# Optimization experiments

Measured on AMD Instinct MI355X. Metric: run time of the kernel, lower is better.

Reference implementation:

```python
import jax, jax.numpy as jnp
import numpy as np

N, H, W, M = 1, 128, 128, 16
HID, STY, CIN, NC, COL = 256, 256, 128, 7, 64


def _lrelu(v):
    return jnp.where(v > 0, v, 0.2 * v)


def _conv(x, w, b=None):
    y = jax.lax.conv_general_dilated(x, w, (1, 1), 'SAME',
                                     dimension_numbers=('NCHW', 'OIHW', 'NCHW'))
    return y if b is None else y + b[None, :, None, None]


def _modlin(f, z, Wt, Wa, ba, Wb, bb):
    # ModLinear, bias=False, mod_bias=True, output_mode=True:
    # y = (f * alpha) @ W^T + beta
    alpha = z @ Wa.T + ba          # [N, in]
    beta = z @ Wb.T + bb           # [N, out]
    return jnp.einsum('nsi,oi->nso', f * alpha[:, None, :], Wt) + beta[:, None, :]


def setup_inputs() -> dict:
    key = jax.random.key(0)
    k = jax.random.split(key, 24)
    s = lambda f: np.float32(1.0 / np.sqrt(f))
    inp = {}
    inp['x'] = jax.random.normal(k[0], (N, H, W, M, CIN), jnp.float32)
    inp['m'] = jax.random.uniform(k[1], (N, H, W, M, NC), jnp.float32)
    inp['z'] = jax.random.normal(k[2], (N, STY), jnp.float32)
    inp['dists'] = jax.random.uniform(k[3], (N, H, W, M), jnp.float32) * 0.05
    # RenderMLP params
    inp['w1'] = jax.random.normal(k[4], (HID, CIN)) * s(CIN)
    inp['b1'] = jnp.zeros((HID,), jnp.float32)
    inp['wma'] = jax.random.normal(k[5], (HID, NC)) * s(NC)
    # 5 stacked ModLinears (fc_2, fc_3, fc_4, fc_5, fc_6)
    inp['ml_w'] = jax.random.normal(k[6], (5, HID, HID)) * s(HID)
    inp['ml_wa'] = jax.random.normal(k[7], (5, HID, STY)) * s(STY)
    inp['ml_ba'] = jnp.ones((5, HID), jnp.float32)
    inp['ml_wb'] = jax.random.normal(k[8], (5, HID, STY)) * s(STY)
    inp['ml_bb'] = jnp.zeros((5, HID), jnp.float32)
    inp['wsig'] = jax.random.normal(k[9], (1, HID)) * s(HID)
    inp['bsig'] = jnp.zeros((1,), jnp.float32)
    inp['wc'] = jax.random.normal(k[10], (COL, HID)) * s(HID)
    inp['bc'] = jnp.zeros((COL,), jnp.float32)
    # RenderCNN params
    inp['wz'] = jax.random.normal(k[11], (4 * HID, STY)) * s(STY)
    inp['bz'] = jnp.zeros((4 * HID,), jnp.float32)
    inp['c1_w'] = jax.random.normal(k[12], (HID, COL, 1, 1)) * s(COL)
    inp['c1_b'] = jnp.zeros((HID,), jnp.float32)
    inp['c2a_w'] = jax.random.normal(k[13], (HID, HID, 3, 3)) * s(HID * 9)
    inp['c2a_b'] = jnp.zeros((HID,), jnp.float32)
    inp['c2b_w'] = jax.random.normal(k[14], (HID, HID, 3, 3)) * s(HID * 9)
    inp['c3a_w'] = jax.random.normal(k[15], (HID, HID, 3, 3)) * s(HID * 9)
    inp['c3a_b'] = jnp.zeros((HID,), jnp.float32)
    inp['c3b_w'] = jax.random.normal(k[16], (HID, HID, 3, 3)) * s(HID * 9)
    inp['c4a_w'] = jax.random.normal(k[17], (HID, HID, 1, 1)) * s(HID)
    inp['c4a_b'] = jnp.zeros((HID,), jnp.float32)
    inp['c4b_w'] = jax.random.normal(k[18], (HID, HID, 1, 1)) * s(HID)
    inp['c4b_b'] = jnp.zeros((HID,), jnp.float32)
    inp['c4_w'] = jax.random.normal(k[19], (3, HID, 1, 1)) * s(HID)
    inp['c4_b'] = jnp.zeros((3,), jnp.float32)
    return inp


def reference(x, m, z, dists, w1, b1, wma, ml_w, ml_wa, ml_ba, ml_wb, ml_bb,
              wsig, bsig, wc, bc, wz, bz, c1_w, c1_b, c2a_w, c2a_b, c2b_w,
              c3a_w, c3a_b, c3b_w, c4a_w, c4a_b, c4b_w, c4b_b, c4_w, c4_b):
    n, h, w_, mm, cin = x.shape
    xf = x.reshape(n, -1, cin)              # [N, S, 128], S = H*W*M
    mf = m.reshape(n, -1, m.shape[-1])      # [N, S, 7]
    # RenderMLP
    f = jnp.einsum('nsi,oi->nso', xf, w1) + b1 + jnp.einsum('nsi,oi->nso', mf, wma)
    f = _lrelu(f)
    for i in range(3):  # fc_2, fc_3, fc_4
        f = _lrelu(_modlin(f, z, ml_w[i], ml_wa[i], ml_ba[i], ml_wb[i], ml_bb[i]))
    sigma = jnp.einsum('nsi,oi->nso', f, wsig) + bsig   # [N, S, 1]
    for i in (3, 4):    # fc_5, fc_6
        f = _lrelu(_modlin(f, z, ml_w[i], ml_wa[i], ml_ba[i], ml_wb[i], ml_bb[i]))
    c = jnp.einsum('nsi,oi->nso', f, wc) + bc           # [N, S, 64]
    # Volumetric alpha compositing along the M ray samples
    sigma = sigma.reshape(n, h, w_, mm)
    c = c.reshape(n, h, w_, mm, -1)
    alpha = 1.0 - jnp.exp(-jax.nn.relu(sigma) * dists)  # [N,H,W,M]
    t = jnp.cumprod(1.0 - alpha + 1e-10, axis=-1)
    t_excl = jnp.concatenate([jnp.ones_like(t[..., :1]), t[..., :-1]], axis=-1)
    wgt = alpha * t_excl
    feat = jnp.einsum('nhwm,nhwmc->nchw', wgt, c)       # [N, 64, H, W]
    # RenderCNN with style modulation
    zc = z @ wz.T + bz
    a0, a1, a2, a3 = jnp.split(zc, 4, axis=-1)
    mod = lambda y, wm, bm: y * (wm[:, :, None, None] + 1.0) + bm[:, :, None, None]
    y = _lrelu(_conv(feat, c1_w, c1_b))
    y = y + _conv(_lrelu(_conv(y, c2a_w, c2a_b)), c2b_w)
    y = _lrelu(mod(y, a0, a1))
    y = y + _conv(_lrelu(_conv(y, c3a_w, c3a_b)), c3b_w)
    y = _lrelu(mod(y, a2, a3))
    y = y + _conv(_lrelu(_conv(y, c4a_w, c4a_b)), c4b_w, c4b_b)
    y = _lrelu(y)
    return _conv(y, c4_w, c4_b)  # [N, 3, H, W]
```

## Files before the change

### kernel.cpp

```cpp
#include <hip/hip_runtime.h>
#include <hip/hip_bf16.h>

#define NPIX 16384
#define S_TOT 262144

typedef __attribute__((ext_vector_type(8))) short bf16x8;
typedef __attribute__((ext_vector_type(4))) float f32x4;

__device__ __forceinline__ float lrelu(float v) { return v > 0.f ? v : 0.2f * v; }
__device__ __forceinline__ unsigned short f2b(float f) {
  unsigned u = __float_as_uint(f);
  return (unsigned short)((u + 0x7FFFu + ((u >> 16) & 1u)) >> 16);
}
__device__ __forceinline__ unsigned pk2(float a, float b) {
  return (unsigned)f2b(a) | ((unsigned)f2b(b) << 16);
}
__device__ __forceinline__ float b2f(short s) {
  return __uint_as_float(((unsigned)(unsigned short)s) << 16);
}
__device__ __forceinline__ float f_lo(int u) { return __uint_as_float((unsigned)u << 16); }
__device__ __forceinline__ float f_hi(int u) { return __uint_as_float((unsigned)u & 0xffff0000u); }

__device__ float g_alpha[5 * 256];
__device__ float g_beta[5 * 256];
__device__ float g_amod[1024];
__device__ float g_sigma[S_TOT];
__device__ float g_c[S_TOT * 64];
__device__ short g_featb[NPIX * 64];
__device__ short g_y1[NPIX * 256];
__device__ short g_y2[NPIX * 256];
__device__ short g_y3[NPIX * 256];
__device__ short g_t [NPIX * 256];
__device__ short g_wpack[385024];
#define O_C1  0
#define O_C2A 16384
#define O_C2B (16384 + 589824)
#define O_C3A (16384 + 2 * 589824)
#define O_C3B (16384 + 3 * 589824)
#define O_C4A (16384 + 4 * 589824)
#define O_C4B (16384 + 4 * 589824 + 65536)
__device__ short g_wpack2[2506752];

__global__ __launch_bounds__(256) void kparams(const float* __restrict__ z,
    const float* __restrict__ wa, const float* __restrict__ ba,
    const float* __restrict__ wb, const float* __restrict__ bb,
    const float* __restrict__ wz, const float* __restrict__ bz) {
  __shared__ float zs[256];
  const int t = threadIdx.x;
  zs[t] = z[t];
  __syncthreads();
  for (int l = 0; l < 5; ++l) {
    float accA = ba[l * 256 + t];
    float accB = bb[l * 256 + t];
    const float* rowA = wa + (l * 256 + t) * 256;
    const float* rowB = wb + (l * 256 + t) * 256;
    for (int k = 0; k < 256; k += 4) {
      float4 va = *(const float4*)(rowA + k);
      float4 vb = *(const float4*)(rowB + k);
      accA += va.x * zs[k] + va.y * zs[k + 1] + va.z * zs[k + 2] + va.w * zs[k + 3];
      accB += vb.x * zs[k] + vb.y * zs[k + 1] + vb.z * zs[k + 2] + vb.w * zs[k + 3];
    }
    g_alpha[l * 256 + t] = accA;
    g_beta[l * 256 + t] = accB;
  }
  for (int j = t; j < 1024; j += 256) {
    float acc = bz[j];
    const float* row = wz + j * 256;
    for (int k = 0; k < 256; k += 4) {
      float4 v = *(const float4*)(row + k);
      acc += v.x * zs[k] + v.y * zs[k + 1] + v.z * zs[k + 2] + v.w * zs[k + 3];
    }
    g_amod[j] = acc;
  }
}

__global__ __launch_bounds__(256) void kprep(
    const float* __restrict__ w1, const float* __restrict__ wma,
    const float* __restrict__ mlw, const float* __restrict__ wc) {
  const int idx = blockIdx.x * 256 + threadIdx.x;
  float val;
  if (idx < 40960) {
    int mt = idx / 2560, r2 = idx % 2560;
    int ks = r2 / 512, r = r2 % 512;
    int ln = r >> 3, j = r & 7;
    int oc = mt * 16 + (ln & 15);
    int k = ks * 32 + (ln >> 4) * 8 + j;
    val = (k < 128) ? w1[oc * 128 + k] : ((k < 135) ? wma[oc * 7 + (k - 128)] : 0.f);
  } else if (idx < 368640) {
    int t = idx - 40960;
    int l = t / 65536, t2 = t % 65536;
    int mt = t2 / 4096, r2 = t2 % 4096;
    int ks = r2 / 512, r = r2 % 512;
    int ln = r >> 3, j = r & 7;
    int oc = mt * 16 + (ln & 15);
    int k = ks * 32 + (ln >> 4) * 8 + j;
    val = mlw[l * 65536 + oc * 256 + k] * g_alpha[l * 256 + k];
  } else {
    int t = idx - 368640;
    int mt = t / 4096, r2 = t % 4096;
    int ks = r2 / 512, r = r2 % 512;
    int ln = r >> 3, j = r & 7;
    int oc = mt * 16 + (ln & 15);
    int k = ks * 32 + (ln >> 4) * 8 + j;
    val = wc[oc * 256 + k];
  }
  g_wpack[idx] = (short)f2b(val);
}

__global__ __launch_bounds__(256) void kprep_cnn(
    const float* __restrict__ c1w,
    const float* __restrict__ c2aw, const float* __restrict__ c2bw,
    const float* __restrict__ c3aw, const float* __restrict__ c3bw,
    const float* __restrict__ c4aw, const float* __restrict__ c4bw) {
  const int idx = blockIdx.x * 256 + threadIdx.x;
  float val;
  if (idx < 16384) {
    int mt = idx / 1024, r2 = idx % 1024;
    int ks = r2 / 512, r = r2 % 512;
    int ln = r >> 3, j = r & 7;
    int oc = mt * 16 + (ln & 15);
    int k = ks * 32 + (ln >> 4) * 8 + j;
    val = c1w[oc * 64 + k];
  } else if (idx < O_C4A) {
    int t = idx - 16384;
    int cv = t / 589824, t2 = t % 589824;
    const float* w = (cv == 0) ? c2aw : (cv == 1) ? c2bw : (cv == 2) ? c3aw : c3bw;
    int mt = t2 / 36864, r2 = t2 % 36864;
    int ks = r2 / 512, r = r2 % 512;
    int ln = r >> 3, j = r & 7;
    int oc = mt * 16 + (ln & 15);
    int k = ks * 32 + (ln >> 4) * 8 + j;
    int tap = k >> 8, ic = k & 255;
    val = w[oc * 2304 + ic * 9 + tap];
  } else {
    int t = idx - O_C4A;
    const float* w = (t < 65536) ? c4aw : c4bw;
    int t2 = t & 65535;
    int mt = t2 / 4096, r2 = t2 % 4096;
    int ks = r2 / 512, r = r2 % 512;
    int ln = r >> 3, j = r & 7;
    int oc = mt * 16 + (ln & 15);
    int k = ks * 32 + (ln >> 4) * 8 + j;
    val = w[oc * 256 + k];
  }
  g_wpack2[idx] = (short)f2b(val);
}

__device__ __forceinline__ bf16x8 ldsB(const short* buf, int s, int kbyte) {
  const char* p = (const char*)buf + s * 512 + (kbyte ^ ((s & 7) << 4));
  return *(const bf16x8*)p;
}

template<int KS>
__device__ __forceinline__ void layer_gemm(const short* __restrict__ gA,
    const short* __restrict__ inb, short* __restrict__ outb,
    const float* __restrict__ bias, int lane, int w) {
  const f32x4 zero = {0.f, 0.f, 0.f, 0.f};
  f32x4 acc[4][4];
#pragma unroll
  for (int mi = 0; mi < 4; ++mi)
#pragma unroll
    for (int ni = 0; ni < 4; ++ni) acc[mi][ni] = zero;
  const int lrow = lane & 15;
  const int lkb = (lane >> 4) * 16;
#pragma unroll
  for (int ks = 0; ks < KS; ++ks) {
    bf16x8 A[4], B[4];
#pragma unroll
    for (int mi = 0; mi < 4; ++mi)
      A[mi] = *(const bf16x8*)(gA + (size_t)((w * 4 + mi) * KS + ks) * 512 + lane * 8);
#pragma unroll
    for (int ni = 0; ni < 4; ++ni)
      B[ni] = ldsB(inb, ni * 16 + lrow, ks * 64 + lkb);
#pragma unroll
    for (int mi = 0; mi < 4; ++mi)
#pragma unroll
      for (int ni = 0; ni < 4; ++ni)
        acc[mi][ni] = __builtin_amdgcn_mfma_f32_16x16x32_bf16(A[mi], B[ni], acc[mi][ni], 0, 0, 0);
  }
  const int rb = (lane >> 4) * 4;
#pragma unroll
  for (int mi = 0; mi < 4; ++mi) {
    const int oc0 = w * 64 + mi * 16 + rb;
    const float b0 = bias[oc0], b1 = bias[oc0 + 1], b2 = bias[oc0 + 2], b3 = bias[oc0 + 3];
#pragma unroll
    for (int ni = 0; ni < 4; ++ni) {
      const int s = ni * 16 + lrow;
      f32x4 a = acc[mi][ni];
      float v0 = lrelu(a[0] + b0), v1 = lrelu(a[1] + b1);
      float v2 = lrelu(a[2] + b2), v3 = lrelu(a[3] + b3);
      char* p = (char*)outb + s * 512 + ((oc0 * 2) ^ ((s & 7) << 4));
      *(int2*)p = make_int2((int)pk2(v0, v1), (int)pk2(v2, v3));
    }
  }
}

__global__ __launch_bounds__(256, 2) void kmlp_mfma(
    const float* __restrict__ x, const float* __restrict__ m_in,
    const float* __restrict__ b1, const float* __restrict__ bc,
    const float* __restrict__ wsig, const float* __restrict__ bsig) {
  __shared__ short fbuf[2][16384];
  __shared__ float bias_all[1600];
  __shared__ float wsig_lds[256];
  __shared__ float sred[256];
  const int tid = threadIdx.x;
  const int lane = tid & 63, w = tid >> 6;
  const int s0 = blockIdx.x * 64;

  {
    const float* xp = x + (size_t)s0 * 128;
    const int s = tid >> 2, c = tid & 3;
#pragma unroll
    for (int e = 0; e < 4; ++e) {
      float4 f0 = *(const float4*)(xp + s * 128 + c * 32 + e * 8);
      float4 f1 = *(const float4*)(xp + s * 128 + c * 32 + e * 8 + 4);
      int4 pk;
      pk.x = (int)pk2(f0.x, f0.y); pk.y = (int)pk2(f0.z, f0.w);
      pk.z = (int)pk2(f1.x, f1.y); pk.w = (int)pk2(f1.z, f1.w);
      char* p = (char*)fbuf[0] + s * 512 + ((c * 64 + e * 16) ^ ((s & 7) << 4));
      *(int4*)p = pk;
    }
  }
  if (tid < 64) {
    const float* mp = m_in + (size_t)(s0 + tid) * 7;
    float mv[8];
#pragma unroll
    for (int q = 0; q < 7; ++q) mv[q] = mp[q];
    mv[7] = 0.f;
    int4 pk;
    pk.x = (int)pk2(mv[0], mv[1]); pk.y = (int)pk2(mv[2], mv[3]);
    pk.z = (int)pk2(mv[4], mv[5]); pk.w = (int)pk2(mv[6], mv[7]);
    char* base = (char*)fbuf[0] + tid * 512;
    const int swz = (tid & 7) << 4;
    *(int4*)(base + (256 ^ swz)) = pk;
    int4 zz = make_int4(0, 0, 0, 0);
    *(int4*)(base + (272 ^ swz)) = zz;
    *(int4*)(base + (288 ^ swz)) = zz;
    *(int4*)(base + (304 ^ swz)) = zz;
  }
  bias_all[tid] = b1[tid];
  for (int i = tid; i < 1280; i += 256) bias_all[256 + i] = g_beta[i];
  if (tid < 64) bias_all[1536 + tid] = bc[tid];
  wsig_lds[tid] = wsig[tid];
  __syncthreads();

  layer_gemm<5>(g_wpack,                     fbuf[0], fbuf[1], bias_all,        lane, w);
  __syncthreads();
  layer_gemm<8>(g_wpack + 40960,             fbuf[1], fbuf[0], bias_all + 256,  lane, w);
  __syncthreads();
  layer_gemm<8>(g_wpack + 40960 + 65536,     fbuf[0], fbuf[1], bias_all + 512,  lane, w);
  __syncthreads();
  layer_gemm<8>(g_wpack + 40960 + 2 * 65536, fbuf[1], fbuf[0], bias_all + 768,  lane, w);
  __syncthreads();
  {
    const int s = tid & 63, q = tid >> 6;
    float part = 0.f;
#pragma unroll
    for (int e = 0; e < 8; ++e) {
      bf16x8 v = ldsB(fbuf[0], s, q * 128 + e * 16);
      const float* wp = wsig_lds + q * 64 + e * 8;
#pragma unroll
      for (int j = 0; j < 8; ++j) part += b2f(v[j]) * wp[j];
    }
    sred[q * 64 + s] = part;
  }
  __syncthreads();
  if (tid < 64)
    g_sigma[s0 + tid] = sred[tid] + sred[64 + tid] + sred[128 + tid] + sred[192 + tid] + bsig[0];
  layer_gemm<8>(g_wpack + 40960 + 3 * 65536, fbuf[0], fbuf[1], bias_all + 1024, lane, w);
  __syncthreads();
  layer_gemm<8>(g_wpack + 40960 + 4 * 65536, fbuf[1], fbuf[0], bias_all + 1280, lane, w);
  __syncthreads();
  {
    const f32x4 zero = {0.f, 0.f, 0.f, 0.f};
    f32x4 acc[4] = {zero, zero, zero, zero};
    const int lrow = lane & 15, lkb = (lane >> 4) * 16;
    const short* gA = g_wpack + 368640;
#pragma unroll
    for (int ks = 0; ks < 8; ++ks) {
      bf16x8 A = *(const bf16x8*)(gA + (size_t)(w * 8 + ks) * 512 + lane * 8);
#pragma unroll
      for (int ni = 0; ni < 4; ++ni) {
        bf16x8 B = ldsB(fbuf[0], ni * 16 + lrow, ks * 64 + lkb);
        acc[ni] = __builtin_amdgcn_mfma_f32_16x16x32_bf16(A, B, acc[ni], 0, 0, 0);
      }
    }
    const int rb = (lane >> 4) * 4;
    const int oc0 = w * 16 + rb;
    const float b0 = bias_all[1536 + oc0], b1v = bias_all[1537 + oc0];
    const float b2v = bias_all[1538 + oc0], b3 = bias_all[1539 + oc0];
#pragma unroll
    for (int ni = 0; ni < 4; ++ni) {
      const int s = ni * 16 + lrow;
      float4 vv;
      vv.x = acc[ni][0] + b0; vv.y = acc[ni][1] + b1v;
      vv.z = acc[ni][2] + b2v; vv.w = acc[ni][3] + b3;
      *(float4*)(g_c + (size_t)(s0 + s) * 64 + oc0) = vv;
    }
  }
}

__global__ __launch_bounds__(256) void kcomposite(const float* __restrict__ dists) {
  const int tid = threadIdx.x;
  const int p = blockIdx.x * 4 + (tid >> 6);
  const int ch = tid & 63;
  const int base = p * 16;
  float T = 1.f, acc = 0.f;
  for (int mm = 0; mm < 16; ++mm) {
    float sgm = g_sigma[base + mm];
    float d = dists[base + mm];
    float a = 1.f - expf(-fmaxf(sgm, 0.f) * d);
    acc += a * T * g_c[(size_t)(base + mm) * 64 + ch];
    T *= (1.f - a + 1e-10f);
  }
  g_featb[p * 64 + ch] = (short)f2b(acc);
}

template<int IC>
__global__ __launch_bounds__(256, 2) void kgemm1x1(const short* __restrict__ in,
    const short* __restrict__ gA, const float* __restrict__ bias,
    const short* __restrict__ res, int domod, const float* __restrict__ modAB,
    short* __restrict__ out) {
  constexpr int KS = IC / 32;
  constexpr int ROWB = IC * 2;
  __shared__ short binb[32 * IC];
  const int tid = threadIdx.x;
  const int lane = tid & 63, w = tid >> 6;
  const int px0 = blockIdx.x * 32;

  for (int e = tid; e < 32 * IC / 8; e += 256) {
    const int px = e / (IC / 8), lg = e % (IC / 8);
    bf16x8 v = *(const bf16x8*)(in + (size_t)(px0 + px) * IC + lg * 8);
    char* p = (char*)binb + px * ROWB + ((lg * 16) ^ ((px & 7) << 4));
    *(bf16x8*)p = v;
  }
  __syncthreads();

  const f32x4 zero = {0.f, 0.f, 0.f, 0.f};
  f32x4 acc[4][2];
#pragma unroll
  for (int mi = 0; mi < 4; ++mi)
#pragma unroll
    for (int ni = 0; ni < 2; ++ni) acc[mi][ni] = zero;
  const int lrow = lane & 15;
  const int lkb = (lane >> 4) * 16;
#pragma unroll
  for (int ks = 0; ks < KS; ++ks) {
    bf16x8 A[4], B[2];
#pragma unroll
    for (int mi = 0; mi < 4; ++mi)
      A[mi] = *(const bf16x8*)(gA + (size_t)((w * 4 + mi) * KS + ks) * 512 + lane * 8);
#pragma unroll
    for (int ni = 0; ni < 2; ++ni) {
      const int s = ni * 16 + lrow;
      const char* p = (const char*)binb + s * ROWB + ((ks * 64 + lkb) ^ ((s & 7) << 4));
      B[ni] = *(const bf16x8*)p;
    }
#pragma unroll
    for (int mi = 0; mi < 4; ++mi)
#pragma unroll
      for (int ni = 0; ni < 2; ++ni)
        acc[mi][ni] = __builtin_amdgcn_mfma_f32_16x16x32_bf16(A[mi], B[ni], acc[mi][ni], 0, 0, 0);
  }
  const int rb = (lane >> 4) * 4;
#pragma unroll
  for (int mi = 0; mi < 4; ++mi) {
    const int oc = w * 64 + mi * 16 + rb;
    float bv[4] = {0.f, 0.f, 0.f, 0.f};
    if (bias) { bv[0] = bias[oc]; bv[1] = bias[oc + 1]; bv[2] = bias[oc + 2]; bv[3] = bias[oc + 3]; }
#pragma unroll
    for (int ni = 0; ni < 2; ++ni) {
      const int gpx = px0 + ni * 16 + lrow;
      f32x4 a = acc[mi][ni];
      float v[4];
#pragma unroll
      for (int r = 0; r < 4; ++r) v[r] = a[r] + bv[r];
      if (res) {
        int2 rv = *(const int2*)(res + (size_t)gpx * 256 + oc);
        v[0] += f_lo(rv.x); v[1] += f_hi(rv.x); v[2] += f_lo(rv.y); v[3] += f_hi(rv.y);
      }
      if (domod) {
#pragma unroll
        for (int r = 0; r < 4; ++r) v[r] = v[r] * (modAB[oc + r] + 1.f) + modAB[256 + oc + r];
      }
#pragma unroll
      for (int r = 0; r < 4; ++r) v[r] = lrelu(v[r]);
      *(int2*)(out + (size_t)gpx * 256 + oc) = make_int2((int)pk2(v[0], v[1]), (int)pk2(v[2], v[3]));
    }
  }
}

__global__ __launch_bounds__(256, 2) void kconv3(const short* __restrict__ in,
    const short* __restrict__ gA, const float* __restrict__ bias,
    const short* __restrict__ res, int domod, const float* __restrict__ modAB,
    short* __restrict__ out) {
  __shared__ short halo[136 * 64];
  const int tid = threadIdx.x;
  const int lane = tid & 63, w = tid >> 6;
  const int oct = blockIdx.x >> 8;
  const int pxt = blockIdx.x & 255;
  const int x0 = (pxt & 3) * 32, y0 = (pxt >> 2) * 2;
  const int oc0 = oct * 128 + w * 32;
  const int lrow = lane & 15;
  const int lkb = (lane >> 4) * 16;

  const f32x4 zero = {0.f, 0.f, 0.f, 0.f};
  f32x4 acc[2][4];
#pragma unroll
  for (int mi = 0; mi < 2; ++mi)
#pragma unroll
    for (int ni = 0; ni < 4; ++ni) acc[mi][ni] = zero;

#pragma unroll 1
  for (int c = 0; c < 4; ++c) {
    for (int e = tid; e < 1088; e += 256) {
      const int row = e >> 3, lg = e & 7;
      const int yy = row / 34, xx = row - yy * 34;
      const int gy = y0 - 1 + yy, gx = x0 - 1 + xx;
      bf16x8 v = {0, 0, 0, 0, 0, 0, 0, 0};
      if (gy >= 0 && gy < 128 && gx >= 0 && gx < 128)
        v = *(const bf16x8*)(in + (size_t)((gy << 7) + gx) * 256 + c * 64 + lg * 8);
      char* p = (char*)halo + row * 128 + ((lg * 16) ^ ((row & 7) << 4));
      *(bf16x8*)p = v;
    }
    __syncthreads();
#pragma unroll
    for (int tap = 0; tap < 9; ++tap) {
      const int ky = tap / 3, kx = tap - ky * 3;
#pragma unroll
      for (int s = 0; s < 2; ++s) {
        const int ksg = tap * 8 + c * 2 + s;
        bf16x8 A[2], B[4];
#pragma unroll
        for (int mi = 0; mi < 2; ++mi)
          A[mi] = *(const bf16x8*)(gA + (size_t)(((oct * 8 + w * 2 + mi) * 72 + ksg)) * 512 + lane * 8);
#pragma unroll
        for (int ni = 0; ni < 4; ++ni) {
          const int p = ni * 16 + lrow;
          const int row = ((p >> 5) + ky) * 34 + (p & 31) + kx;
          const char* bp = (const char*)halo + row * 128 + ((s * 64 + lkb) ^ ((row & 7) << 4));
          B[ni] = *(const bf16x8*)bp;
        }
#pragma unroll
        for (int mi = 0; mi < 2; ++mi)
#pragma unroll
          for (int ni = 0; ni < 4; ++ni)
            acc[mi][ni] = __builtin_amdgcn_mfma_f32_16x16x32_bf16(A[mi], B[ni], acc[mi][ni], 0, 0, 0);
      }
    }
    __syncthreads();
  }

  const int rb = (lane >> 4) * 4;
#pragma unroll
  for (int mi = 0; mi < 2; ++mi) {
    const int oc = oc0 + mi * 16 + rb;
    float bv[4] = {0.f, 0.f, 0.f, 0.f};
    if (bias) { bv[0] = bias[oc]; bv[1] = bias[oc + 1]; bv[2] = bias[oc + 2]; bv[3] = bias[oc + 3]; }
#pragma unroll
    for (int ni = 0; ni < 4; ++ni) {
      const int p = ni * 16 + lrow;
      const int gpx = (y0 + (p >> 5)) * 128 + x0 + (p & 31);
      f32x4 a = acc[mi][ni];
      float v[4];
#pragma unroll
      for (int r = 0; r < 4; ++r) v[r] = a[r] + bv[r];
      if (res) {
        int2 rv = *(const int2*)(res + (size_t)gpx * 256 + oc);
        v[0] += f_lo(rv.x); v[1] += f_hi(rv.x); v[2] += f_lo(rv.y); v[3] += f_hi(rv.y);
      }
      if (domod) {
#pragma unroll
        for (int r = 0; r < 4; ++r) v[r] = v[r] * (modAB[oc + r] + 1.f) + modAB[256 + oc + r];
      }
#pragma unroll
      for (int r = 0; r < 4; ++r) v[r] = lrelu(v[r]);
      *(int2*)(out + (size_t)gpx * 256 + oc) = make_int2((int)pk2(v[0], v[1]), (int)pk2(v[2], v[3]));
    }
  }
}

__global__ __launch_bounds__(256) void kfinal(const short* __restrict__ in,
    const float* __restrict__ w, const float* __restrict__ bias, float* __restrict__ outp) {
  __shared__ float wl[768];
  const int tid = threadIdx.x;
  for (int i = tid; i < 768; i += 256) wl[i] = w[i];
  __syncthreads();
  const int lane = tid & 63;
  const int px = blockIdx.x * 8 + (tid >> 6) * 2 + (lane >> 5);
  const int j = lane & 31;
  bf16x8 v = *(const bf16x8*)(in + (size_t)px * 256 + j * 8);
  float s0 = 0.f, s1 = 0.f, s2 = 0.f;
#pragma unroll
  for (int q = 0; q < 8; ++q) {
    float f = b2f(v[q]);
    s0 += f * wl[j * 8 + q];
    s1 += f * wl[256 + j * 8 + q];
    s2 += f * wl[512 + j * 8 + q];
  }
#pragma unroll
  for (int off = 1; off < 32; off <<= 1) {
    s0 += __shfl_xor(s0, off);
    s1 += __shfl_xor(s1, off);
    s2 += __shfl_xor(s2, off);
  }
  if (j == 0) {
    outp[px] = s0 + bias[0];
    outp[NPIX + px] = s1 + bias[1];
    outp[2 * NPIX + px] = s2 + bias[2];
  }
}

extern "C" void kernel_launch(void* const* d_in, const int* in_sizes, int n_in,
                              void* d_out, int out_size, void* d_ws, size_t ws_size,
                              hipStream_t stream) {
  (void)in_sizes; (void)n_in; (void)out_size; (void)d_ws; (void)ws_size;
  const float* x    = (const float*)d_in[0];
  const float* m    = (const float*)d_in[1];
  const float* z    = (const float*)d_in[2];
  const float* dists= (const float*)d_in[3];
  const float* w1   = (const float*)d_in[4];
  const float* b1   = (const float*)d_in[5];
  const float* wma  = (const float*)d_in[6];
  const float* mlw  = (const float*)d_in[7];
  const float* mlwa = (const float*)d_in[8];
  const float* mlba = (const float*)d_in[9];
  const float* mlwb = (const float*)d_in[10];
  const float* mlbb = (const float*)d_in[11];
  const float* wsig = (const float*)d_in[12];
  const float* bsig = (const float*)d_in[13];
  const float* wc   = (const float*)d_in[14];
  const float* bc   = (const float*)d_in[15];
  const float* wz   = (const float*)d_in[16];
  const float* bz   = (const float*)d_in[17];
  const float* c1w  = (const float*)d_in[18];
  const float* c1b  = (const float*)d_in[19];
  const float* c2aw = (const float*)d_in[20];
  const float* c2ab = (const float*)d_in[21];
  const float* c2bw = (const float*)d_in[22];
  const float* c3aw = (const float*)d_in[23];
  const float* c3ab = (const float*)d_in[24];
  const float* c3bw = (const float*)d_in[25];
  const float* c4aw = (const float*)d_in[26];
  const float* c4ab = (const float*)d_in[27];
  const float* c4bw = (const float*)d_in[28];
  const float* c4bb = (const float*)d_in[29];
  const float* c4w  = (const float*)d_in[30];
  const float* c4b  = (const float*)d_in[31];
  float* outp = (float*)d_out;

  short *pW2, *pFb, *pY1, *pY2, *pY3, *pT;
  float *pAmod;
  hipGetSymbolAddress((void**)&pW2, HIP_SYMBOL(g_wpack2));
  hipGetSymbolAddress((void**)&pFb, HIP_SYMBOL(g_featb));
  hipGetSymbolAddress((void**)&pY1, HIP_SYMBOL(g_y1));
  hipGetSymbolAddress((void**)&pY2, HIP_SYMBOL(g_y2));
  hipGetSymbolAddress((void**)&pY3, HIP_SYMBOL(g_y3));
  hipGetSymbolAddress((void**)&pT,  HIP_SYMBOL(g_t));
  hipGetSymbolAddress((void**)&pAmod, HIP_SYMBOL(g_amod));

  kparams<<<1, 256, 0, stream>>>(z, mlwa, mlba, mlwb, mlbb, wz, bz);
  kprep<<<1504, 256, 0, stream>>>(w1, wma, mlw, wc);
  kprep_cnn<<<9792, 256, 0, stream>>>(c1w, c2aw, c2bw, c3aw, c3bw, c4aw, c4bw);
  kmlp_mfma<<<4096, 256, 0, stream>>>(x, m, b1, bc, wsig, bsig);
  kcomposite<<<4096, 256, 0, stream>>>(dists);
  kgemm1x1<64> <<<512, 256, 0, stream>>>(pFb, pW2 + O_C1,  c1b,  nullptr, 0, nullptr, pY1);
  kconv3<<<512, 256, 0, stream>>>(pY1, pW2 + O_C2A, c2ab, nullptr, 0, nullptr,      pT);
  kconv3<<<512, 256, 0, stream>>>(pT,  pW2 + O_C2B, nullptr, pY1, 1, pAmod,         pY2);
  kconv3<<<512, 256, 0, stream>>>(pY2, pW2 + O_C3A, c3ab, nullptr, 0, nullptr,      pT);
  kconv3<<<512, 256, 0, stream>>>(pT,  pW2 + O_C3B, nullptr, pY2, 1, pAmod + 512,   pY3);
  kgemm1x1<256><<<512, 256, 0, stream>>>(pY3, pW2 + O_C4A, c4ab, nullptr, 0, nullptr, pT);
  kgemm1x1<256><<<512, 256, 0, stream>>>(pT,  pW2 + O_C4B, c4bb, pY3,    0, nullptr, pY1);
  kfinal<<<2048, 256, 0, stream>>>(pY1, c4w, c4b, outp);
}
```

Measured before the change: 632.1 us.

## Fuse final 1x1 convs with output head, store MLP colors as bf16, single-pass conv halo

Several changes land at once. The c4a and c4b 1x1 GEMMs and the final 3-channel projection now run in one kernel that keeps its tiles in LDS, which removes two global round trips and a launch. The per-sample MLP color buffer is stored in bf16 instead of fp32, halving its write and read traffic, at the cost of some precision. The 3x3 conv now loads the full 256-channel halo into a larger LDS buffer once instead of four channel chunks with syncs, trading more LDS per block (lower occupancy) for fewer barriers. Bias arrays are pre-assembled once in kparams, and a wsig weight pack is added that nothing shown uses yet.

```diff
diff --git a/kernel.cpp b/kernel.cpp
--- a/kernel.cpp
+++ b/kernel.cpp
@@ -22,16 +22,16 @@
 __device__ __forceinline__ float f_hi(int u) { return __uint_as_float((unsigned)u & 0xffff0000u); }
 
 __device__ float g_alpha[5 * 256];
-__device__ float g_beta[5 * 256];
+__device__ float g_biasall[1600];
 __device__ float g_amod[1024];
 __device__ float g_sigma[S_TOT];
-__device__ float g_c[S_TOT * 64];
+__device__ short g_c[S_TOT * 64];
 __device__ short g_featb[NPIX * 64];
 __device__ short g_y1[NPIX * 256];
 __device__ short g_y2[NPIX * 256];
 __device__ short g_y3[NPIX * 256];
 __device__ short g_t [NPIX * 256];
-__device__ short g_wpack[385024];
+__device__ short g_wpack[389120];
 #define O_C1  0
 #define O_C2A 16384
 #define O_C2B (16384 + 589824)
@@ -44,11 +44,14 @@
 __global__ __launch_bounds__(256) void kparams(const float* __restrict__ z,
     const float* __restrict__ wa, const float* __restrict__ ba,
     const float* __restrict__ wb, const float* __restrict__ bb,
-    const float* __restrict__ wz, const float* __restrict__ bz) {
+    const float* __restrict__ wz, const float* __restrict__ bz,
+    const float* __restrict__ b1, const float* __restrict__ bc) {
   __shared__ float zs[256];
   const int t = threadIdx.x;
   zs[t] = z[t];
   __syncthreads();
+  g_biasall[t] = b1[t];
+  if (t < 64) g_biasall[1536 + t] = bc[t];
   for (int l = 0; l < 5; ++l) {
     float accA = ba[l * 256 + t];
     float accB = bb[l * 256 + t];
@@ -61,7 +64,7 @@
       accB += vb.x * zs[k] + vb.y * zs[k + 1] + vb.z * zs[k + 2] + vb.w * zs[k + 3];
     }
     g_alpha[l * 256 + t] = accA;
-    g_beta[l * 256 + t] = accB;
+    g_biasall[256 + l * 256 + t] = accB;
   }
   for (int j = t; j < 1024; j += 256) {
     float acc = bz[j];
@@ -76,7 +79,8 @@
 
 __global__ __launch_bounds__(256) void kprep(
     const float* __restrict__ w1, const float* __restrict__ wma,
-    const float* __restrict__ mlw, const float* __restrict__ wc) {
+    const float* __restrict__ mlw, const float* __restrict__ wc,
+    const float* __restrict__ wsig) {
   const int idx = blockIdx.x * 256 + threadIdx.x;
   float val;
   if (idx < 40960) {
@@ -95,7 +99,7 @@
     int oc = mt * 16 + (ln & 15);
     int k = ks * 32 + (ln >> 4) * 8 + j;
     val = mlw[l * 65536 + oc * 256 + k] * g_alpha[l * 256 + k];
-  } else {
+  } else if (idx < 385024) {
     int t = idx - 368640;
     int mt = t / 4096, r2 = t % 4096;
     int ks = r2 / 512, r = r2 % 512;
@@ -103,6 +107,13 @@
     int oc = mt * 16 + (ln & 15);
     int k = ks * 32 + (ln >> 4) * 8 + j;
     val = wc[oc * 256 + k];
+  } else {
+    int t = idx - 385024;
+    int ks = t / 512, r = t % 512;
+    int ln = r >> 3, j = r & 7;
+    int row = ln & 15;
+    int k = ks * 32 + (ln >> 4) * 8 + j;
+    val = (row == 0) ? wsig[k] : 0.f;
   }
   g_wpack[idx] = (short)f2b(val);
 }
@@ -150,6 +161,9 @@
   const char* p = (const char*)buf + s * 512 + (kbyte ^ ((s & 7) << 4));
   return *(const bf16x8*)p;
 }
+__device__ __forceinline__ bf16x8 ldA(const short* gA, int frag, int lane) {
+  return *(const bf16x8*)(gA + ((size_t)frag << 9) + lane * 8);
+}
 
 template<int KS>
 __device__ __forceinline__ void layer_gemm(const short* __restrict__ gA,
@@ -168,7 +182,7 @@
     bf16x8 A[4], B[4];
 #pragma unroll
     for (int mi = 0; mi < 4; ++mi)
-      A[mi] = *(const bf16x8*)(gA + (size_t)((w * 4 + mi) * KS + ks) * 512 + lane * 8);
+      A[mi] = ldA(gA, (w * 4 + mi) * KS + ks, lane);
 #pragma unroll
     for (int ni = 0; ni < 4; ++ni)
       B[ni] = ldsB(inb, ni * 16 + lrow, ks * 64 + lkb);
@@ -197,7 +211,6 @@
 
 __global__ __launch_bounds__(256, 2) void kmlp_mfma(
     const float* __restrict__ x, const float* __restrict__ m_in,
-    const float* __restrict__ b1, const float* __restrict__ bc,
     const float* __restrict__ wsig, const float* __restrict__ bsig) {
   __shared__ short fbuf[2][16384];
   __shared__ float bias_all[1600];
@@ -238,9 +251,7 @@
     *(int4*)(base + (288 ^ swz)) = zz;
     *(int4*)(base + (304 ^ swz)) = zz;
   }
-  bias_all[tid] = b1[tid];
-  for (int i = tid; i < 1280; i += 256) bias_all[256 + i] = g_beta[i];
-  if (tid < 64) bias_all[1536 + tid] = bc[tid];
+  for (int i = tid; i < 1600; i += 256) bias_all[i] = g_biasall[i];
   wsig_lds[tid] = wsig[tid];
   __syncthreads();
 
@@ -278,7 +289,7 @@
     const short* gA = g_wpack + 368640;
 #pragma unroll
     for (int ks = 0; ks < 8; ++ks) {
-      bf16x8 A = *(const bf16x8*)(gA + (size_t)(w * 8 + ks) * 512 + lane * 8);
+      bf16x8 A = ldA(gA, w * 8 + ks, lane);
 #pragma unroll
       for (int ni = 0; ni < 4; ++ni) {
         bf16x8 B = ldsB(fbuf[0], ni * 16 + lrow, ks * 64 + lkb);
@@ -292,10 +303,9 @@
 #pragma unroll
     for (int ni = 0; ni < 4; ++ni) {
       const int s = ni * 16 + lrow;
-      float4 vv;
-      vv.x = acc[ni][0] + b0; vv.y = acc[ni][1] + b1v;
-      vv.z = acc[ni][2] + b2v; vv.w = acc[ni][3] + b3;
-      *(float4*)(g_c + (size_t)(s0 + s) * 64 + oc0) = vv;
+      *(int2*)(g_c + (size_t)(s0 + s) * 64 + oc0) =
+          make_int2((int)pk2(acc[ni][0] + b0, acc[ni][1] + b1v),
+                    (int)pk2(acc[ni][2] + b2v, acc[ni][3] + b3));
     }
   }
 }
@@ -310,7 +320,7 @@
     float sgm = g_sigma[base + mm];
     float d = dists[base + mm];
     float a = 1.f - expf(-fmaxf(sgm, 0.f) * d);
-    acc += a * T * g_c[(size_t)(base + mm) * 64 + ch];
+    acc += a * T * b2f(g_c[(size_t)(base + mm) * 64 + ch]);
     T *= (1.f - a + 1e-10f);
   }
   g_featb[p * 64 + ch] = (short)f2b(acc);
@@ -319,7 +329,6 @@
 template<int IC>
 __global__ __launch_bounds__(256, 2) void kgemm1x1(const short* __restrict__ in,
     const short* __restrict__ gA, const float* __restrict__ bias,
-    const short* __restrict__ res, int domod, const float* __restrict__ modAB,
     short* __restrict__ out) {
   constexpr int KS = IC / 32;
   constexpr int ROWB = IC * 2;
@@ -349,7 +358,7 @@
     bf16x8 A[4], B[2];
 #pragma unroll
     for (int mi = 0; mi < 4; ++mi)
-      A[mi] = *(const bf16x8*)(gA + (size_t)((w * 4 + mi) * KS + ks) * 512 + lane * 8);
+      A[mi] = ldA(gA, (w * 4 + mi) * KS + ks, lane);
 #pragma unroll
     for (int ni = 0; ni < 2; ++ni) {
       const int s = ni * 16 + lrow;
@@ -366,26 +375,14 @@
 #pragma unroll
   for (int mi = 0; mi < 4; ++mi) {
     const int oc = w * 64 + mi * 16 + rb;
-    float bv[4] = {0.f, 0.f, 0.f, 0.f};
-    if (bias) { bv[0] = bias[oc]; bv[1] = bias[oc + 1]; bv[2] = bias[oc + 2]; bv[3] = bias[oc + 3]; }
+    const float4 bv = *(const float4*)(bias + oc);
 #pragma unroll
     for (int ni = 0; ni < 2; ++ni) {
       const int gpx = px0 + ni * 16 + lrow;
       f32x4 a = acc[mi][ni];
-      float v[4];
-#pragma unroll
-      for (int r = 0; r < 4; ++r) v[r] = a[r] + bv[r];
-      if (res) {
-        int2 rv = *(const int2*)(res + (size_t)gpx * 256 + oc);
-        v[0] += f_lo(rv.x); v[1] += f_hi(rv.x); v[2] += f_lo(rv.y); v[3] += f_hi(rv.y);
-      }
-      if (domod) {
-#pragma unroll
-        for (int r = 0; r < 4; ++r) v[r] = v[r] * (modAB[oc + r] + 1.f) + modAB[256 + oc + r];
-      }
-#pragma unroll
-      for (int r = 0; r < 4; ++r) v[r] = lrelu(v[r]);
-      *(int2*)(out + (size_t)gpx * 256 + oc) = make_int2((int)pk2(v[0], v[1]), (int)pk2(v[2], v[3]));
+      float v0 = lrelu(a[0] + bv.x), v1 = lrelu(a[1] + bv.y);
+      float v2 = lrelu(a[2] + bv.z), v3 = lrelu(a[3] + bv.w);
+      *(int2*)(out + (size_t)gpx * 256 + oc) = make_int2((int)pk2(v0, v1), (int)pk2(v2, v3));
     }
   }
 }
@@ -394,7 +391,7 @@
     const short* __restrict__ gA, const float* __restrict__ bias,
     const short* __restrict__ res, int domod, const float* __restrict__ modAB,
     short* __restrict__ out) {
-  __shared__ short halo[136 * 64];
+  __shared__ short halo[136 * 256];
   const int tid = threadIdx.x;
   const int lane = tid & 63, w = tid >> 6;
   const int oct = blockIdx.x >> 8;
@@ -404,6 +401,18 @@
   const int lrow = lane & 15;
   const int lkb = (lane >> 4) * 16;
 
+  for (int e = tid; e < 4352; e += 256) {
+    const int row = e >> 5, lg = e & 31;
+    const int yy = row / 34, xx = row - yy * 34;
+    const int gy = y0 - 1 + yy, gx = x0 - 1 + xx;
+    bf16x8 v = {0, 0, 0, 0, 0, 0, 0, 0};
+    if (gy >= 0 && gy < 128 && gx >= 0 && gx < 128)
+      v = *(const bf16x8*)(in + (size_t)((gy << 7) + gx) * 256 + lg * 8);
+    char* p = (char*)halo + row * 512 + ((lg * 16) ^ ((row & 7) << 4));
+    *(bf16x8*)p = v;
+  }
+  __syncthreads();
+
   const f32x4 zero = {0.f, 0.f, 0.f, 0.f};
   f32x4 acc[2][4];
 #pragma unroll
@@ -411,44 +420,29 @@
 #pragma unroll
     for (int ni = 0; ni < 4; ++ni) acc[mi][ni] = zero;
 
-#pragma unroll 1
-  for (int c = 0; c < 4; ++c) {
-    for (int e = tid; e < 1088; e += 256) {
-      const int row = e >> 3, lg = e & 7;
-      const int yy = row / 34, xx = row - yy * 34;
-      const int gy = y0 - 1 + yy, gx = x0 - 1 + xx;
-      bf16x8 v = {0, 0, 0, 0, 0, 0, 0, 0};
-      if (gy >= 0 && gy < 128 && gx >= 0 && gx < 128)
-        v = *(const bf16x8*)(in + (size_t)((gy << 7) + gx) * 256 + c * 64 + lg * 8);
-      char* p = (char*)halo + row * 128 + ((lg * 16) ^ ((row & 7) << 4));
-      *(bf16x8*)p = v;
-    }
-    __syncthreads();
-#pragma unroll
-    for (int tap = 0; tap < 9; ++tap) {
-      const int ky = tap / 3, kx = tap - ky * 3;
-#pragma unroll
-      for (int s = 0; s < 2; ++s) {
-        const int ksg = tap * 8 + c * 2 + s;
-        bf16x8 A[2], B[4];
-#pragma unroll
-        for (int mi = 0; mi < 2; ++mi)
-          A[mi] = *(const bf16x8*)(gA + (size_t)(((oct * 8 + w * 2 + mi) * 72 + ksg)) * 512 + lane * 8);
-#pragma unroll
-        for (int ni = 0; ni < 4; ++ni) {
-          const int p = ni * 16 + lrow;
-          const int row = ((p >> 5) + ky) * 34 + (p & 31) + kx;
-          const char* bp = (const char*)halo + row * 128 + ((s * 64 + lkb) ^ ((row & 7) << 4));
-          B[ni] = *(const bf16x8*)bp;
-        }
-#pragma unroll
-        for (int mi = 0; mi < 2; ++mi)
-#pragma unroll
-          for (int ni = 0; ni < 4; ++ni)
-            acc[mi][ni] = __builtin_amdgcn_mfma_f32_16x16x32_bf16(A[mi], B[ni], acc[mi][ni], 0, 0, 0);
+#pragma unroll
+  for (int tap = 0; tap < 9; ++tap) {
+    const int ky = tap / 3, kx = tap - ky * 3;
+#pragma unroll
+    for (int s = 0; s < 8; ++s) {
+      const int ksg = tap * 8 + s;
+      bf16x8 A[2], B[4];
+#pragma unroll
+      for (int mi = 0; mi < 2; ++mi)
+        A[mi] = ldA(gA, (oct * 8 + w * 2 + mi) * 72 + ksg, lane);
+#pragma unroll
+      for (int ni = 0; ni < 4; ++ni) {
+        const int p = ni * 16 + lrow;
+        const int row = ((p >> 5) + ky) * 34 + (p & 31) + kx;
+        const char* bp = (const char*)halo + row * 512 + ((s * 64 + lkb) ^ ((row & 7) << 4));
+        B[ni] = *(const bf16x8*)bp;
       }
-    }
-    __syncthreads();
+#pragma unroll
+      for (int mi = 0; mi < 2; ++mi)
+#pragma unroll
+        for (int ni = 0; ni < 4; ++ni)
+          acc[mi][ni] = __builtin_amdgcn_mfma_f32_16x16x32_bf16(A[mi], B[ni], acc[mi][ni], 0, 0, 0);
+    }
   }
 
   const int rb = (lane >> 4) * 4;
@@ -480,34 +474,108 @@
   }
 }
 
-__global__ __launch_bounds__(256) void kfinal(const short* __restrict__ in,
-    const float* __restrict__ w, const float* __restrict__ bias, float* __restrict__ outp) {
+__device__ __forceinline__ void fuse_gemm(const short* __restrict__ inb,
+    const short* __restrict__ gA, const float* __restrict__ bias,
+    const short* __restrict__ resb, short* __restrict__ outb, int lane, int w) {
+  const f32x4 zero = {0.f, 0.f, 0.f, 0.f};
+  f32x4 acc[4][2];
+#pragma unroll
+  for (int mi = 0; mi < 4; ++mi)
+#pragma unroll
+    for (int ni = 0; ni < 2; ++ni) acc[mi][ni] = zero;
+  const int lrow = lane & 15;
+  const int lkb = (lane >> 4) * 16;
+#pragma unroll
+  for (int ks = 0; ks < 8; ++ks) {
+    bf16x8 A[4], B[2];
+#pragma unroll
+    for (int mi = 0; mi < 4; ++mi)
+      A[mi] = ldA(gA, (w * 4 + mi) * 8 + ks, lane);
+#pragma unroll
+    for (int ni = 0; ni < 2; ++ni)
+      B[ni] = ldsB(inb, ni * 16 + lrow, ks * 64 + lkb);
+#pragma unroll
+    for (int mi = 0; mi < 4; ++mi)
+#pragma unroll
+      for (int ni = 0; ni < 2; ++ni)
+        acc[mi][ni] = __builtin_amdgcn_mfma_f32_16x16x32_bf16(A[mi], B[ni], acc[mi][ni], 0, 0, 0);
+  }
+  const int rb = (lane >> 4) * 4;
+#pragma unroll
+  for (int mi = 0; mi < 4; ++mi) {
+    const int oc = w * 64 + mi * 16 + rb;
+    const float4 bv = *(const float4*)(bias + oc);
+#pragma unroll
+    for (int ni = 0; ni < 2; ++ni) {
+      const int s = ni * 16 + lrow;
+      f32x4 a = acc[mi][ni];
+      float v[4] = {a[0] + bv.x, a[1] + bv.y, a[2] + bv.z, a[3] + bv.w};
+      if (resb) {
+        const char* rp = (const char*)resb + s * 512 + ((oc * 2) ^ ((s & 7) << 4));
+        int2 rv = *(const int2*)rp;
+        v[0] += f_lo(rv.x); v[1] += f_hi(rv.x); v[2] += f_lo(rv.y); v[3] += f_hi(rv.y);
+      }
+#pragma unroll
+      for (int r = 0; r < 4; ++r) v[r] = lrelu(v[r]);
+      char* p = (char*)outb + s * 512 + ((oc * 2) ^ ((s & 7) << 4));
+      *(int2*)p = make_int2((int)pk2(v[0], v[1]), (int)pk2(v[2], v[3]));
+    }
+  }
+}
+
+__global__ __launch_bounds__(256, 2) void kc4fuse(const short* __restrict__ y3,
+    const short* __restrict__ gA4a, const short* __restrict__ gA4b,
+    const float* __restrict__ c4ab, const float* __restrict__ c4bb,
+    const float* __restrict__ c4w, const float* __restrict__ c4b,
+    float* __restrict__ outp) {
+  __shared__ short binb[32 * 256];
+  __shared__ short tb[32 * 256];
+  __shared__ short yb[32 * 256];
   __shared__ float wl[768];
+  __shared__ float sred3[768];
   const int tid = threadIdx.x;
-  for (int i = tid; i < 768; i += 256) wl[i] = w[i];
-  __syncthreads();
-  const int lane = tid & 63;
-  const int px = blockIdx.x * 8 + (tid >> 6) * 2 + (lane >> 5);
-  const int j = lane & 31;
-  bf16x8 v = *(const bf16x8*)(in + (size_t)px * 256 + j * 8);
-  float s0 = 0.f, s1 = 0.f, s2 = 0.f;
-#pragma unroll
-  for (int q = 0; q < 8; ++q) {
-    float f = b2f(v[q]);
-    s0 += f * wl[j * 8 + q];
-    s1 += f * wl[256 + j * 8 + q];
-    s2 += f * wl[512 + j * 8 + q];
-  }
-#pragma unroll
-  for (int off = 1; off < 32; off <<= 1) {
-    s0 += __shfl_xor(s0, off);
-    s1 += __shfl_xor(s1, off);
-    s2 += __shfl_xor(s2, off);
-  }
-  if (j == 0) {
-    outp[px] = s0 + bias[0];
-    outp[NPIX + px] = s1 + bias[1];
-    outp[2 * NPIX + px] = s2 + bias[2];
+  const int lane = tid & 63, w = tid >> 6;
+  const int px0 = blockIdx.x * 32;
+
+  for (int e = tid; e < 1024; e += 256) {
+    const int px = e >> 5, lg = e & 31;
+    bf16x8 v = *(const bf16x8*)(y3 + (size_t)(px0 + px) * 256 + lg * 8);
+    char* p = (char*)binb + px * 512 + ((lg * 16) ^ ((px & 7) << 4));
+    *(bf16x8*)p = v;
+  }
+  for (int i = tid; i < 768; i += 256) wl[i] = c4w[i];
+  __syncthreads();
+
+  fuse_gemm(binb, gA4a, c4ab, nullptr, tb, lane, w);
+  __syncthreads();
+  fuse_gemm(tb, gA4b, c4bb, binb, yb, lane, w);
+  __syncthreads();
+
+  {
+    const int px = tid >> 3, g = tid & 7;
+    float s0 = 0.f, s1 = 0.f, s2 = 0.f;
+#pragma unroll
+    for (int e = 0; e < 4; ++e) {
+      bf16x8 v = ldsB(yb, px, g * 64 + e * 16);
+      const int ic0 = g * 32 + e * 8;
+#pragma unroll
+      for (int j = 0; j < 8; ++j) {
+        float f = b2f(v[j]);
+        s0 += f * wl[ic0 + j];
+        s1 += f * wl[256 + ic0 + j];
+        s2 += f * wl[512 + ic0 + j];
+      }
+    }
+    sred3[px * 8 + g] = s0;
+    sred3[256 + px * 8 + g] = s1;
+    sred3[512 + px * 8 + g] = s2;
+  }
+  __syncthreads();
+  if (tid < 96) {
+    const int och = tid >> 5, px = tid & 31;
+    const float* sp = sred3 + och * 256 + px * 8;
+    float s = sp[0] + sp[1] + sp[2] + sp[3] + sp[4] + sp[5] + sp[6] + sp[7];
+    outp[och * NPIX + px0 + px] = s + c4b[och];
   }
 }
 
@@ -559,17 +627,15 @@
   hipGetSymbolAddress((void**)&pT,  HIP_SYMBOL(g_t));
   hipGetSymbolAddress((void**)&pAmod, HIP_SYMBOL(g_amod));
 
-  kparams<<<1, 256, 0, stream>>>(z, mlwa, mlba, mlwb, mlbb, wz, bz);
-  kprep<<<1504, 256, 0, stream>>>(w1, wma, mlw, wc);
+  kparams<<<1, 256, 0, stream>>>(z, mlwa, mlba, mlwb, mlbb, wz, bz, b1, bc);
+  kprep<<<1520, 256, 0, stream>>>(w1, wma, mlw, wc, wsig);
   kprep_cnn<<<9792, 256, 0, stream>>>(c1w, c2aw, c2bw, c3aw, c3bw, c4aw, c4bw);
-  kmlp_mfma<<<4096, 256, 0, stream>>>(x, m, b1, bc, wsig, bsig);
+  kmlp_mfma<<<4096, 256, 0, stream>>>(x, m, wsig, bsig);
   kcomposite<<<4096, 256, 0, stream>>>(dists);
-  kgemm1x1<64> <<<512, 256, 0, stream>>>(pFb, pW2 + O_C1,  c1b,  nullptr, 0, nullptr, pY1);
-  kconv3<<<512, 256, 0, stream>>>(pY1, pW2 + O_C2A, c2ab, nullptr, 0, nullptr,      pT);
-  kconv3<<<512, 256, 0, stream>>>(pT,  pW2 + O_C2B, nullptr, pY1, 1, pAmod,         pY2);
-  kconv3<<<512, 256, 0, stream>>>(pY2, pW2 + O_C3A, c3ab, nullptr, 0, nullptr,      pT);
-  kconv3<<<512, 256, 0, stream>>>(pT,  pW2 + O_C3B, nullptr, pY2, 1, pAmod + 512,   pY3);
-  kgemm1x1<256><<<512, 256, 0, stream>>>(pY3, pW2 + O_C4A, c4ab, nullptr, 0, nullptr, pT);
-  kgemm1x1<256><<<512, 256, 0, stream>>>(pT,  pW2 + O_C4B, c4bb, pY3,    0, nullptr, pY1);
-  kfinal<<<2048, 256, 0, stream>>>(pY1, c4w, c4b, outp);
-}
+  kgemm1x1<64> <<<512, 256, 0, stream>>>(pFb, pW2 + O_C1, c1b, pY1);
+  kconv3<<<512, 256, 0, stream>>>(pY1, pW2 + O_C2A, c2ab, nullptr, 0, nullptr,    pT);
+  kconv3<<<512, 256, 0, stream>>>(pT,  pW2 + O_C2B, nullptr, pY1, 1, pAmod,       pY2);
+  kconv3<<<512, 256, 0, stream>>>(pY2, pW2 + O_C3A, c3ab, nullptr, 0, nullptr,    pT);
+  kconv3<<<512, 256, 0, stream>>>(pT,  pW2 + O_C3B, nullptr, pY2, 1, pAmod + 512, pY3);
+  kc4fuse<<<512, 256, 0, stream>>>(pY3, pW2 + O_C4A, pW2 + O_C4B, c4ab, c4bb, c4w, c4b, outp);
+}
```

New measurement: 615.2 us. -2.7%, faster.
